# Kernel optimization log

Measured on AMD Instinct MI355X. Metric: run time of the kernel, lower is better.

## Reference

```python
import jax, jax.numpy as jnp
import numpy as np

HEADS = 16
DIM_HEAD = 64
DIM = 1024
EPS = 1e-5


def _layernorm(x, g, b):
    mu = jnp.mean(x, axis=-1, keepdims=True)
    var = jnp.var(x, axis=-1, keepdims=True)
    return (x - mu) * jax.lax.rsqrt(var + EPS) * g + b


def setup_inputs() -> dict:
    key = jax.random.key(0)
    ks = jax.random.split(key, 8)
    inner = HEADS * DIM_HEAD  # 1024
    x = jax.random.normal(ks[0], (2, 2048, DIM), dtype=jnp.float32)
    w_qkv = jax.random.normal(ks[1], (DIM, inner * 3), dtype=jnp.float32) * (DIM ** -0.5)
    w_out = jax.random.normal(ks[2], (inner, DIM), dtype=jnp.float32) * (inner ** -0.5)
    ln1_g = jnp.ones((DIM,), jnp.float32)
    ln1_b = jnp.zeros((DIM,), jnp.float32)
    ln2_g = jnp.ones((DIM,), jnp.float32)
    ln2_b = jnp.zeros((DIM,), jnp.float32)
    return {"x": x, "ln1_g": ln1_g, "ln1_b": ln1_b, "w_qkv": w_qkv,
            "w_out": w_out, "ln2_g": ln2_g, "ln2_b": ln2_b}


def reference(x, ln1_g, ln1_b, w_qkv, w_out, ln2_g, ln2_b):
    b, n, _ = x.shape
    scale = DIM_HEAD ** -0.5
    xn = _layernorm(x, ln1_g, ln1_b)
    qkv = xn @ w_qkv  # [b, n, 3*inner]
    q, k, v = jnp.split(qkv, 3, axis=-1)
    # b n (h d) -> b h n d
    resh = lambda t: t.reshape(b, n, HEADS, DIM_HEAD).transpose(0, 2, 1, 3)
    q, k, v = resh(q) * scale, resh(k), resh(v)
    sim = jnp.einsum('bhid,bhjd->bhij', q, k)
    causal = jnp.tril(jnp.ones((n, n), dtype=bool))
    # masked_fill(triu(1), 0) followed by relu == relu masked to lower triangle
    attn = jnp.where(causal, jax.nn.relu(sim), 0.0)
    out = jnp.einsum('bhij,bhjd->bhid', attn, v)
    out = out.transpose(0, 2, 1, 3).reshape(b, n, HEADS * DIM_HEAD)
    return _layernorm(out @ w_out, ln2_g, ln2_b)
```

## Files before the change

kernel.cpp:

```cpp
#include <hip/hip_runtime.h>
#include <cstdint>
#include <cstddef>


typedef __bf16 bf16_t;
typedef __bf16 bf16x8 __attribute__((ext_vector_type(8)));
typedef __bf16 bf16x4 __attribute__((ext_vector_type(4)));
typedef float  f32x4  __attribute__((ext_vector_type(4)));

#define DEV_INLINE __device__ __forceinline__

DEV_INLINE void async_copy16(void* lds, const void* g) {
  __builtin_amdgcn_global_load_lds(
      (__attribute__((address_space(1))) void*)(g),
      (__attribute__((address_space(3))) void*)(lds), 16, 0, 0);
}

__global__ __launch_bounds__(256) void prep_kernel(
    const float* __restrict__ x, const float* __restrict__ g1,
    const float* __restrict__ b1, bf16_t* __restrict__ xn,
    const float* __restrict__ w_qkv, bf16_t* __restrict__ wqkvT,
    const float* __restrict__ w_out, bf16_t* __restrict__ woutT) {
  const int bid = blockIdx.x;
  const int t = threadIdx.x;
  if (bid < 4096) {
    const int w = t >> 6, l = t & 63;
    const float* xr = x + (size_t)bid * 1024;
    float4 v = *(const float4*)(xr + t * 4);
    float s  = v.x + v.y + v.z + v.w;
    float s2 = v.x * v.x + v.y * v.y + v.z * v.z + v.w * v.w;
    #pragma unroll
    for (int off = 32; off >= 1; off >>= 1) {
      s  += __shfl_down(s, off);
      s2 += __shfl_down(s2, off);
    }
    __shared__ float red[8];
    if (l == 0) { red[w] = s; red[4 + w] = s2; }
    __syncthreads();
    s  = red[0] + red[1] + red[2] + red[3];
    s2 = red[4] + red[5] + red[6] + red[7];
    float mu  = s * (1.0f / 1024.0f);
    float var = s2 * (1.0f / 1024.0f) - mu * mu;
    float rs  = rsqrtf(var + 1e-5f);
    float4 gv = *(const float4*)(g1 + t * 4);
    float4 bv = *(const float4*)(b1 + t * 4);
    bf16x4 o;
    o[0] = (bf16_t)((v.x - mu) * rs * gv.x + bv.x);
    o[1] = (bf16_t)((v.y - mu) * rs * gv.y + bv.y);
    o[2] = (bf16_t)((v.z - mu) * rs * gv.z + bv.z);
    o[3] = (bf16_t)((v.w - mu) * rs * gv.w + bv.w);
    *(bf16x4*)(xn + (size_t)bid * 1024 + t * 4) = o;
  } else {
    const float* wsrc; bf16_t* wdst; int N, tile;
    if (bid < 4864) { wsrc = w_qkv; wdst = wqkvT; N = 3072; tile = bid - 4096; }
    else            { wsrc = w_out; wdst = woutT; N = 1024; tile = bid - 4864; }
    const int ntiles = N >> 6;
    const int n0 = (tile % ntiles) * 64, k0 = (tile / ntiles) * 64;
    __shared__ __align__(16) float tl[64][68];
    #pragma unroll
    for (int c = 0; c < 4; ++c) {
      int idx = c * 256 + t;
      int r = idx >> 4, c4 = (idx & 15) * 4;
      *(float4*)&tl[r][c4] = *(const float4*)(wsrc + (size_t)(k0 + r) * N + n0 + c4);
    }
    __syncthreads();
    #pragma unroll
    for (int c = 0; c < 2; ++c) {
      int idx = c * 256 + t;
      int nl = idx >> 3, kc = (idx & 7) * 8;
      bf16x8 o;
      #pragma unroll
      for (int ii = 0; ii < 8; ++ii) o[ii] = (bf16_t)tl[kc + ii][nl];
      *(bf16x8*)(wdst + (size_t)(n0 + nl) * 1024 + k0 + kc) = o;
    }
  }
}

__global__ __launch_bounds__(256) void ln2_kernel(
    const bf16_t* __restrict__ z0, const bf16_t* __restrict__ z1,
    const float* __restrict__ g, const float* __restrict__ bta,
    float* __restrict__ out) {
  const int row = blockIdx.x;
  const int t = threadIdx.x, w = t >> 6, l = t & 63;
  bf16x4 a0 = *(const bf16x4*)(z0 + (size_t)row * 1024 + t * 4);
  bf16x4 a1 = *(const bf16x4*)(z1 + (size_t)row * 1024 + t * 4);
  float4 v;
  v.x = (float)a0[0] + (float)a1[0];
  v.y = (float)a0[1] + (float)a1[1];
  v.z = (float)a0[2] + (float)a1[2];
  v.w = (float)a0[3] + (float)a1[3];
  float s  = v.x + v.y + v.z + v.w;
  float s2 = v.x * v.x + v.y * v.y + v.z * v.z + v.w * v.w;
  #pragma unroll
  for (int off = 32; off >= 1; off >>= 1) {
    s  += __shfl_down(s, off);
    s2 += __shfl_down(s2, off);
  }
  __shared__ float red[8];
  if (l == 0) { red[w] = s; red[4 + w] = s2; }
  __syncthreads();
  s  = red[0] + red[1] + red[2] + red[3];
  s2 = red[4] + red[5] + red[6] + red[7];
  float mu  = s * (1.0f / 1024.0f);
  float var = s2 * (1.0f / 1024.0f) - mu * mu;
  float rs  = rsqrtf(var + 1e-5f);
  float4 gv = *(const float4*)(g + t * 4);
  float4 bv = *(const float4*)(bta + t * 4);
  float4 o;
  o.x = (v.x - mu) * rs * gv.x + bv.x;
  o.y = (v.y - mu) * rs * gv.y + bv.y;
  o.z = (v.z - mu) * rs * gv.z + bv.z;
  o.w = (v.w - mu) * rs * gv.w + bv.w;
  *(float4*)(out + (size_t)row * 1024 + t * 4) = o;
}

template <int EPI, int KSPLIT>
__global__ __launch_bounds__(256, 3) void gemm128_kernel(
    const bf16_t* __restrict__ A, const bf16_t* __restrict__ Bt,
    void* __restrict__ C0, void* __restrict__ C1, void* __restrict__ C2) {
  __shared__ __align__(16) bf16_t As[128 * 64];
  __shared__ __align__(16) bf16_t Bs[128 * 64];
  const int t = threadIdx.x;
  const int w = t >> 6, l = t & 63, l15 = l & 15, quad = l >> 4;
  const int wy = w >> 1, wx = w & 1;
  const int m0 = blockIdx.y * 128, n0 = blockIdx.x * 128;
  const int kz = (KSPLIT > 1) ? blockIdx.z : 0;
  const int kt0 = kz * (16 / KSPLIT), kt1 = kt0 + (16 / KSPLIT);

  const int r_l = l >> 3;
  const int u_src = (l & 7) ^ r_l;
  const int rswz = l15 & 7;

  f32x4 acc[4][4];
  #pragma unroll
  for (int i = 0; i < 4; ++i)
    #pragma unroll
    for (int j = 0; j < 4; ++j) acc[i][j] = (f32x4)0.0f;

  for (int kt = kt0; kt < kt1; ++kt) {
    __syncthreads();
    #pragma unroll
    for (int c = 0; c < 4; ++c) {
      int idx = w * 4 + c;
      int row = idx * 8 + r_l;
      async_copy16(&As[idx * 512], A + (size_t)(m0 + row) * 1024 + kt * 64 + u_src * 8);
      async_copy16(&Bs[idx * 512], Bt + (size_t)(n0 + row) * 1024 + kt * 64 + u_src * 8);
    }
    __syncthreads();
    #pragma unroll
    for (int kk = 0; kk < 2; ++kk) {
      bf16x8 af[4], bfr[4];
      #pragma unroll
      for (int i = 0; i < 4; ++i)
        af[i] = *(const bf16x8*)&As[(wy * 64 + i * 16 + l15) * 64 + (((kk * 4 + quad) ^ rswz) * 8)];
      #pragma unroll
      for (int j = 0; j < 4; ++j)
        bfr[j] = *(const bf16x8*)&Bs[(wx * 64 + j * 16 + l15) * 64 + (((kk * 4 + quad) ^ rswz) * 8)];
      #pragma unroll
      for (int i = 0; i < 4; ++i)
        #pragma unroll
        for (int j = 0; j < 4; ++j)
          acc[i][j] = __builtin_amdgcn_mfma_f32_16x16x32_bf16(af[i], bfr[j], acc[i][j], 0, 0, 0);
    }
  }

  if (EPI == 0) {
    bf16_t* C = (bf16_t*)(kz == 0 ? C0 : C1);
    #pragma unroll
    for (int i = 0; i < 4; ++i)
      #pragma unroll
      for (int j = 0; j < 4; ++j)
        #pragma unroll
        for (int r = 0; r < 4; ++r) {
          int m = m0 + wy * 64 + i * 16 + quad * 4 + r;
          int n = n0 + wx * 64 + j * 16 + l15;
          C[(size_t)m * 1024 + n] = (bf16_t)acc[i][j][r];
        }
  } else {
    int nb = n0 + wx * 64;
    int which = nb >> 10;
    int head = (nb & 1023) >> 6;
    const int bq = m0 >> 11;
    const int mb = (m0 & 2047) + wy * 64;
    if (which == 2) {
      bf16_t* dst = (bf16_t*)C2 + ((size_t)(bq * 16 + head)) * 64 * 2048;
      #pragma unroll
      for (int i = 0; i < 4; ++i)
        #pragma unroll
        for (int j = 0; j < 4; ++j) {
          bf16x4 pk;
          #pragma unroll
          for (int r = 0; r < 4; ++r) pk[r] = (bf16_t)acc[i][j][r];
          int d = j * 16 + l15;
          int pos = mb + i * 16 + quad * 4;
          *(bf16x4*)(dst + (size_t)d * 2048 + pos) = pk;
        }
    } else {
      bf16_t* dst = which == 0 ? (bf16_t*)C0 : (bf16_t*)C1;
      float sc = which == 0 ? 0.125f : 1.0f;
      #pragma unroll
      for (int i = 0; i < 4; ++i)
        #pragma unroll
        for (int j = 0; j < 4; ++j)
          #pragma unroll
          for (int r = 0; r < 4; ++r) {
            int pos = mb + i * 16 + quad * 4 + r;
            int d = j * 16 + l15;
            dst[(((size_t)(bq * 16 + head)) * 2048 + pos) * 64 + d] =
                (bf16_t)(acc[i][j][r] * sc);
          }
    }
  }
}

__global__ __launch_bounds__(256, 2) void attn_kernel(
    const bf16_t* __restrict__ q, const bf16_t* __restrict__ k,
    const bf16_t* __restrict__ vT, bf16_t* __restrict__ out) {
  __shared__ __align__(16) bf16_t Ks[2][64 * 64];
  __shared__ __align__(16) bf16_t Vts[2][64 * 64];
  __shared__ __align__(16) bf16_t Ss[4][2][16 * 72];

  const int x = blockIdx.x, h = blockIdx.y, b = blockIdx.z;
  const int m = ((x & 1) == 0) ? (x >> 1) : 15 - (x >> 1);
  const int t = threadIdx.x;
  const int w = t >> 6, l = t & 63, l15 = l & 15, quad = l >> 4;
  const size_t bh = (size_t)(b * 16 + h);
  const int r_lo = m, r_hi = 31 - m;
  const int niter = 32 - m;

  const int r_l = l >> 3;
  const int u_g = (l & 7) ^ r_l;
  const int rswz = l15 & 7;

  auto stage_tile = [&](int buf, int kt) {
    #pragma unroll
    for (int c = 0; c < 4; ++c) {
      int op = w * 4 + c;
      int mK = op >> 3;
      int idx = op & 7;
      int row = idx * 8 + r_l;
      if (mK == 0)
        async_copy16(&Ks[buf][idx * 512],
                     k + (bh * 2048 + kt * 64 + row) * 64 + u_g * 8);
      else
        async_copy16(&Vts[buf][idx * 512],
                     vT + (bh * 64 + row) * 2048 + kt * 64 + u_g * 8);
    }
  };

  auto load_lds = [&](const bf16_t* Kb, const bf16_t* Vb,
                      bf16x8 (&bk)[2][4], bf16x8 (&bv)[2][4]) {
    #pragma unroll
    for (int kk = 0; kk < 2; ++kk)
      #pragma unroll
      for (int tj = 0; tj < 4; ++tj) {
        int u = ((kk * 4 + quad) ^ rswz) * 8;
        bk[kk][tj] = *(const bf16x8*)&Kb[(tj * 16 + l15) * 64 + u];
        bv[kk][tj] = *(const bf16x8*)&Vb[(tj * 16 + l15) * 64 + u];
      }
  };

  bf16x8 qa[2][2];
  {
    #pragma unroll
    for (int kk = 0; kk < 2; ++kk) {
      qa[0][kk] = *(const bf16x8*)(q + (bh * 2048 + r_lo * 64 + w * 16 + l15) * 64 + kk * 32 + quad * 8);
      qa[1][kk] = *(const bf16x8*)(q + (bh * 2048 + r_hi * 64 + w * 16 + l15) * 64 + kk * 32 + quad * 8);
    }
  }

  f32x4 acc0[4], acc1[4];
  #pragma unroll
  for (int tj = 0; tj < 4; ++tj) { acc0[tj] = (f32x4)0.0f; acc1[tj] = (f32x4)0.0f; }

  auto sU = [&](f32x4 (&sacc)[4], bf16x8 (&qf)[2], bf16x8 (&bk)[2][4]) {
    #pragma unroll
    for (int tj = 0; tj < 4; ++tj) sacc[tj] = (f32x4)0.0f;
    #pragma unroll
    for (int kk = 0; kk < 2; ++kk)
      #pragma unroll
      for (int tj = 0; tj < 4; ++tj)
        sacc[tj] = __builtin_amdgcn_mfma_f32_16x16x32_bf16(bk[kk][tj], qf[kk], sacc[tj], 0, 0, 0);
  };
  auto wU = [&](f32x4 (&sacc)[4], bool dg, bf16_t* SsBuf) {
    #pragma unroll
    for (int tj = 0; tj < 4; ++tj) {
      bf16x4 pk;
      #pragma unroll
      for (int r = 0; r < 4; ++r) {
        float v = fmaxf(sacc[tj][r], 0.0f);
        if (dg && (tj * 16 + quad * 4 + r > w * 16 + l15)) v = 0.0f;
        pk[r] = (bf16_t)v;
      }
      *(bf16x4*)&SsBuf[l15 * 72 + tj * 16 + quad * 4] = pk;
    }
  };
  auto pU = [&](f32x4 (&accr)[4], bf16x8 (&bv)[2][4], const bf16_t* SsBuf) {
    #pragma unroll
    for (int kk = 0; kk < 2; ++kk) {
      bf16x8 as_ = *(const bf16x8*)&SsBuf[l15 * 72 + kk * 32 + quad * 8];
      #pragma unroll
      for (int tj = 0; tj < 4; ++tj)
        accr[tj] = __builtin_amdgcn_mfma_f32_16x16x32_bf16(bv[kk][tj], as_, accr[tj], 0, 0, 0);
    }
  };

  bf16_t* SsA = &Ss[w][0][0];
  bf16_t* SsB = &Ss[w][1][0];

  stage_tile(0, 0);
  for (int kt = 0; kt < niter; ++kt) {
    __syncthreads();
    if (kt + 1 < niter) stage_tile((kt + 1) & 1, kt + 1);
    const int buf = kt & 1;
    bf16x8 bk[2][4], bv[2][4];
    load_lds(Ks[buf], Vts[buf], bk, bv);
    if (kt <= r_lo) {
      f32x4 s0[4], s1[4];
      sU(s0, qa[0], bk);
      sU(s1, qa[1], bk);
      wU(s0, kt == r_lo, SsA);
      wU(s1, kt == r_hi, SsB);
      pU(acc0, bv, SsA);
      pU(acc1, bv, SsB);
    } else {
      f32x4 s1[4];
      sU(s1, qa[1], bk);
      wU(s1, kt == r_hi, SsB);
      pU(acc1, bv, SsB);
    }
  }

  #pragma unroll
  for (int tj = 0; tj < 4; ++tj) {
    bf16x4 p0, p1;
    #pragma unroll
    for (int r = 0; r < 4; ++r) { p0[r] = (bf16_t)acc0[tj][r]; p1[r] = (bf16_t)acc1[tj][r]; }
    int posA = r_lo * 64 + w * 16 + l15;
    int posB = r_hi * 64 + w * 16 + l15;
    int col = h * 64 + tj * 16 + quad * 4;
    *(bf16x4*)(out + ((size_t)b * 2048 + posA) * 1024 + col) = p0;
    *(bf16x4*)(out + ((size_t)b * 2048 + posB) * 1024 + col) = p1;
  }
}

extern "C" void kernel_launch(void* const* d_in, const int* in_sizes, int n_in,
                              void* d_out, int out_size, void* d_ws, size_t ws_size,
                              hipStream_t stream) {
  (void)in_sizes; (void)n_in; (void)out_size; (void)ws_size;
  const float* x     = (const float*)d_in[0];
  const float* ln1_g = (const float*)d_in[1];
  const float* ln1_b = (const float*)d_in[2];
  const float* w_qkv = (const float*)d_in[3];
  const float* w_out = (const float*)d_in[4];
  const float* ln2_g = (const float*)d_in[5];
  const float* ln2_b = (const float*)d_in[6];
  float* out = (float*)d_out;

  char* ws = (char*)d_ws;
  bf16_t* xn     = (bf16_t*)(ws + 0);
  bf16_t* wqkvT  = (bf16_t*)(ws + 8388608);
  bf16_t* woutT  = (bf16_t*)(ws + 14680064);
  bf16_t* qb     = (bf16_t*)(ws + 16777216);
  bf16_t* kb     = (bf16_t*)(ws + 25165824);
  bf16_t* vTb    = (bf16_t*)(ws + 41943040);
  bf16_t* ao     = (bf16_t*)(ws + 50331648);
  bf16_t* zb0    = (bf16_t*)(ws + 58720256);
  bf16_t* zb1    = (bf16_t*)(ws + 67108864);

  prep_kernel<<<5120, 256, 0, stream>>>(x, ln1_g, ln1_b, xn, w_qkv, wqkvT, w_out, woutT);
  gemm128_kernel<1, 1><<<dim3(24, 32), 256, 0, stream>>>(xn, wqkvT, qb, kb, vTb);
  attn_kernel<<<dim3(16, 16, 2), 256, 0, stream>>>(qb, kb, vTb, ao);
  gemm128_kernel<0, 2><<<dim3(8, 32, 2), 256, 0, stream>>>(ao, woutT, zb0, zb1, nullptr);
  ln2_kernel<<<4096, 256, 0, stream>>>(zb0, zb1, ln2_g, ln2_b, out);
}
```

Measured before the change: 187.9 us.

## Split attention over key ranges with fp32 atomic accumulation and conversion pass

The attention kernel now pairs adjacent query tiles and splits each pair's key range into chunks of up to 8 tiles, launching 40 blocks per head instead of 16. Partial outputs are combined with fp32 atomicAdd into a zeroed buffer, and a new conversion kernel turns that buffer into bf16 for the output projection. The goal is more parallelism and better load balance across CUs. In exchange it adds atomics, a zero-fill inside prep, an extra kernel launch and extra memory traffic; the fp32 buffer also reuses the workspace region of zb0/zb1, which is safe only because the conversion finishes before the projection GEMM writes there.

After: 285.0 us. 1.52x slower.

```diff
diff --git a/kernel.cpp b/kernel.cpp
--- a/kernel.cpp
+++ b/kernel.cpp
@@ -20,13 +20,16 @@
     const float* __restrict__ x, const float* __restrict__ g1,
     const float* __restrict__ b1, bf16_t* __restrict__ xn,
     const float* __restrict__ w_qkv, bf16_t* __restrict__ wqkvT,
-    const float* __restrict__ w_out, bf16_t* __restrict__ woutT) {
+    const float* __restrict__ w_out, bf16_t* __restrict__ woutT,
+    float* __restrict__ ob32) {
   const int bid = blockIdx.x;
   const int t = threadIdx.x;
   if (bid < 4096) {
     const int w = t >> 6, l = t & 63;
     const float* xr = x + (size_t)bid * 1024;
     float4 v = *(const float4*)(xr + t * 4);
+    float4 z; z.x = 0.0f; z.y = 0.0f; z.z = 0.0f; z.w = 0.0f;
+    *(float4*)(ob32 + (size_t)bid * 1024 + t * 4) = z;
     float s  = v.x + v.y + v.z + v.w;
     float s2 = v.x * v.x + v.y * v.y + v.z * v.z + v.w * v.w;
     #pragma unroll
@@ -76,6 +79,16 @@
   }
 }
 
+__global__ __launch_bounds__(256) void cvt_kernel(
+    const float* __restrict__ ob32, bf16_t* __restrict__ ao) {
+  const int row = blockIdx.x;
+  const int t = threadIdx.x;
+  float4 v = *(const float4*)(ob32 + (size_t)row * 1024 + t * 4);
+  bf16x4 o;
+  o[0] = (bf16_t)v.x; o[1] = (bf16_t)v.y; o[2] = (bf16_t)v.z; o[3] = (bf16_t)v.w;
+  *(bf16x4*)(ao + (size_t)row * 1024 + t * 4) = o;
+}
+
 __global__ __launch_bounds__(256) void ln2_kernel(
     const bf16_t* __restrict__ z0, const bf16_t* __restrict__ z1,
     const float* __restrict__ g, const float* __restrict__ bta,
@@ -213,20 +226,26 @@
   }
 }
 
-__global__ __launch_bounds__(256, 2) void attn_kernel(
+__global__ __launch_bounds__(256, 3) void attn_kernel(
     const bf16_t* __restrict__ q, const bf16_t* __restrict__ k,
-    const bf16_t* __restrict__ vT, bf16_t* __restrict__ out) {
+    const bf16_t* __restrict__ vT, float* __restrict__ oacc) {
   __shared__ __align__(16) bf16_t Ks[2][64 * 64];
   __shared__ __align__(16) bf16_t Vts[2][64 * 64];
   __shared__ __align__(16) bf16_t Ss[4][2][16 * 72];
 
-  const int x = blockIdx.x, h = blockIdx.y, b = blockIdx.z;
-  const int m = ((x & 1) == 0) ? (x >> 1) : 15 - (x >> 1);
+  const int h = blockIdx.x, c = blockIdx.y, b = blockIdx.z;
+  int a, i;
+  if (c < 4)       { a = c;                i = 0; }
+  else if (c < 12) { int e = c - 4;  a = 4 + (e >> 1); i = e & 1; }
+  else if (c < 24) { int e = c - 12; int d3 = e / 3; a = 8 + d3; i = e - d3 * 3; }
+  else             { int e = c - 24; a = 12 + (e >> 2); i = e & 3; }
+  const int kt_lo = 8 * i;
+  const int kt_hi = min(8 * i + 8, 2 * a + 2);
+  const int rA = 2 * a, rB = 2 * a + 1;
+
   const int t = threadIdx.x;
   const int w = t >> 6, l = t & 63, l15 = l & 15, quad = l >> 4;
   const size_t bh = (size_t)(b * 16 + h);
-  const int r_lo = m, r_hi = 31 - m;
-  const int niter = 32 - m;
 
   const int r_l = l >> 3;
   const int u_g = (l & 7) ^ r_l;
@@ -234,8 +253,8 @@
 
   auto stage_tile = [&](int buf, int kt) {
     #pragma unroll
-    for (int c = 0; c < 4; ++c) {
-      int op = w * 4 + c;
+    for (int cc = 0; cc < 4; ++cc) {
+      int op = w * 4 + cc;
       int mK = op >> 3;
       int idx = op & 7;
       int row = idx * 8 + r_l;
@@ -264,8 +283,8 @@
   {
     #pragma unroll
     for (int kk = 0; kk < 2; ++kk) {
-      qa[0][kk] = *(const bf16x8*)(q + (bh * 2048 + r_lo * 64 + w * 16 + l15) * 64 + kk * 32 + quad * 8);
-      qa[1][kk] = *(const bf16x8*)(q + (bh * 2048 + r_hi * 64 + w * 16 + l15) * 64 + kk * 32 + quad * 8);
+      qa[0][kk] = *(const bf16x8*)(q + (bh * 2048 + rA * 64 + w * 16 + l15) * 64 + kk * 32 + quad * 8);
+      qa[1][kk] = *(const bf16x8*)(q + (bh * 2048 + rB * 64 + w * 16 + l15) * 64 + kk * 32 + quad * 8);
     }
   }
 
@@ -308,40 +327,41 @@
   bf16_t* SsA = &Ss[w][0][0];
   bf16_t* SsB = &Ss[w][1][0];
 
-  stage_tile(0, 0);
-  for (int kt = 0; kt < niter; ++kt) {
-    __syncthreads();
-    if (kt + 1 < niter) stage_tile((kt + 1) & 1, kt + 1);
-    const int buf = kt & 1;
+  stage_tile(0, kt_lo);
+  for (int kt = kt_lo; kt < kt_hi; ++kt) {
+    __syncthreads();
+    if (kt + 1 < kt_hi) stage_tile((kt + 1 - kt_lo) & 1, kt + 1);
+    const int buf = (kt - kt_lo) & 1;
     bf16x8 bk[2][4], bv[2][4];
     load_lds(Ks[buf], Vts[buf], bk, bv);
-    if (kt <= r_lo) {
+    if (kt < rB) {
       f32x4 s0[4], s1[4];
       sU(s0, qa[0], bk);
       sU(s1, qa[1], bk);
-      wU(s0, kt == r_lo, SsA);
-      wU(s1, kt == r_hi, SsB);
+      wU(s0, kt == rA, SsA);
+      wU(s1, false, SsB);
       pU(acc0, bv, SsA);
       pU(acc1, bv, SsB);
     } else {
       f32x4 s1[4];
       sU(s1, qa[1], bk);
-      wU(s1, kt == r_hi, SsB);
+      wU(s1, true, SsB);
       pU(acc1, bv, SsB);
     }
   }
 
+  const int posA = rA * 64 + w * 16 + l15;
+  const int posB = rB * 64 + w * 16 + l15;
+  float* baseA = oacc + ((size_t)b * 2048 + posA) * 1024 + h * 64;
+  float* baseB = oacc + ((size_t)b * 2048 + posB) * 1024 + h * 64;
   #pragma unroll
-  for (int tj = 0; tj < 4; ++tj) {
-    bf16x4 p0, p1;
-    #pragma unroll
-    for (int r = 0; r < 4; ++r) { p0[r] = (bf16_t)acc0[tj][r]; p1[r] = (bf16_t)acc1[tj][r]; }
-    int posA = r_lo * 64 + w * 16 + l15;
-    int posB = r_hi * 64 + w * 16 + l15;
-    int col = h * 64 + tj * 16 + quad * 4;
-    *(bf16x4*)(out + ((size_t)b * 2048 + posA) * 1024 + col) = p0;
-    *(bf16x4*)(out + ((size_t)b * 2048 + posB) * 1024 + col) = p1;
-  }
+  for (int tj = 0; tj < 4; ++tj)
+    #pragma unroll
+    for (int r = 0; r < 4; ++r) {
+      int d = tj * 16 + quad * 4 + r;
+      atomicAdd(baseA + d, acc0[tj][r]);
+      atomicAdd(baseB + d, acc1[tj][r]);
+    }
 }
 
 extern "C" void kernel_launch(void* const* d_in, const int* in_sizes, int n_in,
@@ -365,12 +385,14 @@
   bf16_t* kb     = (bf16_t*)(ws + 25165824);
   bf16_t* vTb    = (bf16_t*)(ws + 41943040);
   bf16_t* ao     = (bf16_t*)(ws + 50331648);
+  float*  ob32   = (float*) (ws + 58720256);
   bf16_t* zb0    = (bf16_t*)(ws + 58720256);
   bf16_t* zb1    = (bf16_t*)(ws + 67108864);
 
-  prep_kernel<<<5120, 256, 0, stream>>>(x, ln1_g, ln1_b, xn, w_qkv, wqkvT, w_out, woutT);
+  prep_kernel<<<5120, 256, 0, stream>>>(x, ln1_g, ln1_b, xn, w_qkv, wqkvT, w_out, woutT, ob32);
   gemm128_kernel<1, 1><<<dim3(24, 32), 256, 0, stream>>>(xn, wqkvT, qb, kb, vTb);
-  attn_kernel<<<dim3(16, 16, 2), 256, 0, stream>>>(qb, kb, vTb, ao);
+  attn_kernel<<<dim3(16, 40, 2), 256, 0, stream>>>(qb, kb, vTb, ob32);
+  cvt_kernel<<<4096, 256, 0, stream>>>(ob32, ao);
   gemm128_kernel<0, 2><<<dim3(8, 32, 2), 256, 0, stream>>>(ao, woutT, zb0, zb1, nullptr);
   ln2_kernel<<<4096, 256, 0, stream>>>(zb0, zb1, ln2_g, ln2_b, out);
 }
```
